# Optimization experiments

Hardware: AMD Instinct MI355X
Metric: run time of the kernel (lower is better)

Reference implementation:

```python
import jax, jax.numpy as jnp
import numpy as np

EMB_K = 512
EMB_DIM = 256
BETA = 0.25
GAMMA = 0.99
EPS = 1e-5
B, T = 16, 4096


def setup_inputs() -> dict:
    key = jax.random.key(0)
    k1, k2, k3 = jax.random.split(key, 3)
    return {
        "inputs": jax.random.normal(k1, (B, EMB_DIM, T), dtype=jnp.float32),
        "emb_weight": jax.random.normal(k2, (EMB_K, EMB_DIM), dtype=jnp.float32),
        "ema_w": jax.random.normal(k3, (EMB_K, EMB_DIM), dtype=jnp.float32),
        "ema_cluster_size": jnp.zeros((EMB_K,), dtype=jnp.float32),
    }


def reference(inputs, emb_weight, ema_w, ema_cluster_size):
    # [B, D, T] -> [B, T, D]
    x = jnp.transpose(inputs, (0, 2, 1))
    flat = x.reshape(-1, EMB_DIM)  # [N, D]

    # squared euclidean distances to codebook: [N, K]
    dist = (jnp.sum(flat * flat, axis=1, keepdims=True)
            + jnp.sum(emb_weight * emb_weight, axis=1)
            - 2.0 * flat @ emb_weight.T)
    idx = jnp.argmin(dist, axis=1)            # [N]
    enc = jax.nn.one_hot(idx, EMB_K, dtype=flat.dtype)  # [N, K]

    # --- EMA codebook update (training branch) ---
    counts = jax.ops.segment_sum(jnp.ones_like(idx, dtype=flat.dtype), idx,
                                 num_segments=EMB_K)  # == enc.sum(0)
    new_cs = ema_cluster_size * GAMMA + (1.0 - GAMMA) * counts
    n = jnp.sum(new_cs)
    new_cs = (new_cs + EPS) / (n + EMB_K * EPS) * n
    dw = jax.ops.segment_sum(flat, idx, num_segments=EMB_K)  # == enc.T @ flat
    new_ema_w = ema_w * GAMMA + (1.0 - GAMMA) * dw
    new_emb_weight = new_ema_w / new_cs[:, None]

    # quantize with updated codebook (gather == enc @ new_emb_weight)
    Q = new_emb_weight[idx].reshape(x.shape)  # [B, T, D]

    e_latent_loss = jnp.mean((jax.lax.stop_gradient(Q) - x) ** 2)
    loss = BETA * e_latent_loss

    # straight-through
    Q_st = x + jax.lax.stop_gradient(Q - x)

    avg_probs = jnp.mean(enc, axis=0)
    PP = jnp.exp(-jnp.sum(avg_probs * jnp.log(avg_probs + 1e-10)))

    return loss, jnp.transpose(Q_st, (0, 2, 1)), PP, enc
```

## Files before the change

### kernel.cpp

```cpp
#include <hip/hip_runtime.h>

#define N_TOT 65536
#define DIM 256
#define KK 512
#define TT 4096
#define BB 16

typedef short bf16x8 __attribute__((ext_vector_type(8)));
typedef float f32x4 __attribute__((ext_vector_type(4)));

__device__ __forceinline__ ushort f2bf(float f) {
    unsigned u = __float_as_uint(f);
    unsigned r = (u + 0x7fffu + ((u >> 16) & 1u)) >> 16;
    return (ushort)r;
}

__global__ void k_se(const float* __restrict__ emb, float* __restrict__ se) {
    int wid = threadIdx.x >> 6, lane = threadIdx.x & 63;
    int k = blockIdx.x * 4 + wid;
    const float4* e4 = (const float4*)emb;
    float4 v = e4[k * 64 + lane];
    float s = v.x * v.x + v.y * v.y + v.z * v.z + v.w * v.w;
#pragma unroll
    for (int m = 1; m < 64; m <<= 1) s += __shfl_xor(s, m);
    if (lane == 0) se[k] = s;
}

__global__ void k_split_e(const float* __restrict__ emb, ushort* __restrict__ eb) {
    int k = blockIdx.x, tid = threadIdx.x;
    int c0 = tid * 4;
    float4 v = *(const float4*)(emb + k * DIM + c0);
    float f[4] = {v.x, v.y, v.z, v.w};
    ushort h[4], l[4];
#pragma unroll
    for (int j = 0; j < 4; ++j) {
        h[j] = f2bf(f[j]);
        float hf = __uint_as_float(((unsigned)h[j]) << 16);
        l[j] = f2bf(f[j] - hf);
    }
    uint2 hp = make_uint2((unsigned)h[0] | ((unsigned)h[1] << 16),
                          (unsigned)h[2] | ((unsigned)h[3] << 16));
    uint2 lp = make_uint2((unsigned)l[0] | ((unsigned)l[1] << 16),
                          (unsigned)l[2] | ((unsigned)l[3] << 16));
    *(uint2*)(eb + (size_t)k * 512 + c0) = hp;
    *(uint2*)(eb + (size_t)k * 512 + 256 + c0) = lp;
}

__global__ __launch_bounds__(256) void k_split_x(const float* __restrict__ in,
                                                 ushort* __restrict__ xt) {
    __shared__ float ls[64][65];
    int tid = threadIdx.x;
    int b = blockIdx.x >> 8;
    int rest = blockIdx.x & 255;
    int tt = rest >> 2, dt = rest & 3;
    int t0 = tt * 64, d0 = dt * 64;
    int tl = tid & 63, dg = tid >> 6;
    const float* src = in + (size_t)b * DIM * TT + t0 + tl;
#pragma unroll
    for (int p = 0; p < 16; ++p) {
        int d = dg * 16 + p;
        ls[d][tl] = src[(size_t)(d0 + d) * TT];
    }
    __syncthreads();
    int c0 = dg * 16;
    int n = b * TT + t0 + tl;
    ushort* row = xt + (size_t)n * 512;
    ushort h[16], l[16];
#pragma unroll
    for (int j = 0; j < 16; ++j) {
        float v = ls[c0 + j][tl];
        h[j] = f2bf(v);
        float hf = __uint_as_float(((unsigned)h[j]) << 16);
        l[j] = f2bf(v - hf);
    }
    uint hu[8], lu[8];
#pragma unroll
    for (int j = 0; j < 8; ++j) {
        hu[j] = (unsigned)h[2 * j] | ((unsigned)h[2 * j + 1] << 16);
        lu[j] = (unsigned)l[2 * j] | ((unsigned)l[2 * j + 1] << 16);
    }
    *(uint4*)(row + d0 + c0) = make_uint4(hu[0], hu[1], hu[2], hu[3]);
    *(uint4*)(row + d0 + c0 + 8) = make_uint4(hu[4], hu[5], hu[6], hu[7]);
    *(uint4*)(row + 256 + d0 + c0) = make_uint4(lu[0], lu[1], lu[2], lu[3]);
    *(uint4*)(row + 256 + d0 + c0 + 8) = make_uint4(lu[4], lu[5], lu[6], lu[7]);
}

__global__ void k_zero(float* __restrict__ dw, unsigned* __restrict__ counts,
                       unsigned* __restrict__ lossd) {
    int i = blockIdx.x * 256 + threadIdx.x;
    if (i < 131072) dw[i] = 0.f;
    int j = i - 131072;
    if (j >= 0 && j < 512) counts[j] = 0u;
    if (j >= 512 && j < 514) lossd[j - 512] = 0u;
}

__global__ __launch_bounds__(256) void k_dist(
    const ushort* __restrict__ xt, const ushort* __restrict__ eb,
    const float* __restrict__ se,
    float* __restrict__ partd, int* __restrict__ parti) {
    __shared__ ushort As[128 * 64];
    __shared__ ushort Bs[128 * 64];
    const int tid = threadIdx.x;
    const int lane = tid & 63, w = tid >> 6;
    const int bj = blockIdx.x, bi = blockIdx.y;
    const int n0 = bi * 128, k0 = bj * 128;
    const int wr = w >> 1, wc = w & 1;

    f32x4 acc[4][4] = {};

    for (int it = 0; it < 12; ++it) {
        const int region = it >> 2, sub = it & 3;
        const int aoff = (region == 2 ? 256 : 0) + sub * 64;
        const int boff = (region == 1 ? 256 : 0) + sub * 64;
#pragma unroll
        for (int i = 0; i < 4; ++i) {
            int r = i * 32 + w * 8 + (lane >> 3);
            int slot = (lane & 7) ^ (r & 7);
            const ushort* ga = xt + (size_t)(n0 + r) * 512 + aoff + slot * 8;
            const ushort* gb = eb + (size_t)(k0 + r) * 512 + boff + slot * 8;
            __builtin_amdgcn_global_load_lds(
                (const __attribute__((address_space(1))) void*)ga,
                (__attribute__((address_space(3))) void*)&As[(size_t)(i * 256 + w * 64) * 8],
                16, 0, 0);
            __builtin_amdgcn_global_load_lds(
                (const __attribute__((address_space(1))) void*)gb,
                (__attribute__((address_space(3))) void*)&Bs[(size_t)(i * 256 + w * 64) * 8],
                16, 0, 0);
        }
        __syncthreads();
#pragma unroll
        for (int kk = 0; kk < 2; ++kk) {
            bf16x8 af[4], bfr[4];
#pragma unroll
            for (int mi = 0; mi < 4; ++mi) {
                int row = wr * 64 + mi * 16 + (lane & 15);
                int slot = (kk * 4 + (lane >> 4)) ^ (row & 7);
                af[mi] = *(const bf16x8*)&As[row * 64 + slot * 8];
            }
#pragma unroll
            for (int ni = 0; ni < 4; ++ni) {
                int row = wc * 64 + ni * 16 + (lane & 15);
                int slot = (kk * 4 + (lane >> 4)) ^ (row & 7);
                bfr[ni] = *(const bf16x8*)&Bs[row * 64 + slot * 8];
            }
#pragma unroll
            for (int mi = 0; mi < 4; ++mi)
#pragma unroll
                for (int ni = 0; ni < 4; ++ni)
                    acc[mi][ni] = __builtin_amdgcn_mfma_f32_16x16x32_bf16(
                        af[mi], bfr[ni], acc[mi][ni], 0, 0, 0);
        }
        __syncthreads();
    }

    float* pd = (float*)As;
    int* pi = (int*)Bs;
#pragma unroll
    for (int mi = 0; mi < 4; ++mi) {
#pragma unroll
        for (int j = 0; j < 4; ++j) {
            int r = wr * 64 + mi * 16 + (lane >> 4) * 4 + j;
            float dmin = 3.4e38f;
            int bidx = 0x7fffffff;
#pragma unroll
            for (int ni = 0; ni < 4; ++ni) {
                int k = k0 + wc * 64 + ni * 16 + (lane & 15);
                float dv = fmaf(-2.f, acc[mi][ni][j], se[k]);
                if (dv < dmin) { dmin = dv; bidx = k; }
            }
            pd[r * 32 + wc * 16 + (lane & 15)] = dmin;
            pi[r * 32 + wc * 16 + (lane & 15)] = bidx;
        }
    }
    __syncthreads();
    if (tid < 128) {
        float dmin = 3.4e38f;
        int bidx = 0x7fffffff;
        for (int c = 0; c < 32; ++c) {
            float dv = pd[tid * 32 + c];
            int iv = pi[tid * 32 + c];
            if (dv < dmin || (dv == dmin && iv < bidx)) { dmin = dv; bidx = iv; }
        }
        partd[(size_t)bj * N_TOT + n0 + tid] = dmin;
        parti[(size_t)bj * N_TOT + n0 + tid] = bidx;
    }
}

__global__ void k_combine(const float* __restrict__ partd, const int* __restrict__ parti,
                          int* __restrict__ idx, unsigned* __restrict__ counts) {
    __shared__ unsigned h[512];
    int tid = threadIdx.x;
    h[tid] = 0u;
    h[tid + 256] = 0u;
    __syncthreads();
    int n = blockIdx.x * 256 + tid;
    float dmin = 3.4e38f;
    int bidx = 0x7fffffff;
#pragma unroll
    for (int p = 0; p < 4; ++p) {
        float dv = partd[(size_t)p * N_TOT + n];
        int iv = parti[(size_t)p * N_TOT + n];
        if (dv < dmin || (dv == dmin && iv < bidx)) { dmin = dv; bidx = iv; }
    }
    idx[n] = bidx;
    atomicAdd(&h[bidx], 1u);
    __syncthreads();
    if (h[tid]) atomicAdd(&counts[tid], h[tid]);
    if (h[tid + 256]) atomicAdd(&counts[tid + 256], h[tid + 256]);
}

__global__ void k_enc_zero(float2* __restrict__ enc2) {
    size_t base = (size_t)blockIdx.x * (256 * 32) + threadIdx.x;
#pragma unroll
    for (int j = 0; j < 32; ++j) enc2[base + j * 256] = make_float2(0.f, 0.f);
}

__global__ void k_enc_ones(const int* __restrict__ idx, float* __restrict__ enc) {
    int n = blockIdx.x * 256 + threadIdx.x;
    enc[(size_t)n * KK + idx[n]] = 1.0f;
}

__global__ void k_scalars(const unsigned* __restrict__ counts, const float* __restrict__ cs_in,
                          float* __restrict__ csn, float* __restrict__ pp_out,
                          unsigned* __restrict__ cursor) {
    __shared__ float red[512];
    __shared__ unsigned sc[512];
    int k = threadIdx.x;
    unsigned ci = counts[k];
    float c = (float)ci;
    float pre = cs_in[k] * 0.99f + 0.01f * c;
    red[k] = pre;
    sc[k] = ci;
    __syncthreads();
#pragma unroll
    for (int s = 256; s > 0; s >>= 1) {
        if (k < s) red[k] += red[k + s];
        __syncthreads();
    }
    float nsum = red[0];
    __syncthreads();
    csn[k] = (pre + 1e-5f) / (nsum + 512 * 1e-5f) * nsum;
    float p = c * (1.0f / 65536.f);
    red[k] = -p * logf(p + 1e-10f);
    __syncthreads();
#pragma unroll
    for (int s = 256; s > 0; s >>= 1) {
        if (k < s) red[k] += red[k + s];
        __syncthreads();
    }
    if (k == 0) pp_out[0] = expf(red[0]);
#pragma unroll
    for (int s = 1; s < 512; s <<= 1) {
        unsigned v = (k >= s) ? sc[k - s] : 0u;
        __syncthreads();
        sc[k] += v;
        __syncthreads();
    }
    cursor[k] = sc[k] - ci;
}

__global__ void k_scatter(const int* __restrict__ idx, unsigned* __restrict__ cursor,
                          unsigned* __restrict__ sortedp) {
    int n = blockIdx.x * 256 + threadIdx.x;
    int k = idx[n];
    unsigned p = atomicAdd(&cursor[k], 1u);
    sortedp[p] = (unsigned)n | ((unsigned)k << 17);
}

__global__ __launch_bounds__(256) void k_dwsum(const ushort* __restrict__ xt,
                                               const unsigned* __restrict__ sortedp,
                                               float* __restrict__ dw) {
    int gw = blockIdx.x * 4 + (threadIdx.x >> 6);
    int lane = threadIdx.x & 63;
    int base = gw * 16;
    unsigned pk[16];
#pragma unroll
    for (int i = 0; i < 16; ++i) pk[i] = sortedp[base + i];
    float acc[8] = {0.f, 0.f, 0.f, 0.f, 0.f, 0.f, 0.f, 0.f};
    int curk = (int)(pk[0] >> 17);
#pragma unroll
    for (int i = 0; i < 16; ++i) {
        int n = (int)(pk[i] & 0x1ffffu);
        int k = (int)(pk[i] >> 17);
        if (k != curk) {
#pragma unroll
            for (int j = 0; j < 8; ++j) {
                float other = __shfl(acc[j], lane + 32);
                if (lane < 32) atomicAdd(&dw[curk * DIM + lane * 8 + j], acc[j] + other);
                acc[j] = 0.f;
            }
            curk = k;
        }
        uint4 v = *(const uint4*)(xt + (size_t)n * 512 + lane * 8);
        unsigned u[4] = {v.x, v.y, v.z, v.w};
#pragma unroll
        for (int j = 0; j < 4; ++j) {
            acc[2 * j] += __uint_as_float(u[j] << 16);
            acc[2 * j + 1] += __uint_as_float(u[j] & 0xffff0000u);
        }
    }
#pragma unroll
    for (int j = 0; j < 8; ++j) {
        float other = __shfl(acc[j], lane + 32);
        if (lane < 32) atomicAdd(&dw[curk * DIM + lane * 8 + j], acc[j] + other);
    }
}

__global__ void k_newemb(const float* __restrict__ ema_w, const float* __restrict__ dw,
                         const float* __restrict__ csn, float* __restrict__ newemb) {
    int i = blockIdx.x * 256 + threadIdx.x;
    int k = i >> 8;
    newemb[i] = (ema_w[i] * 0.99f + 0.01f * dw[i]) / csn[k];
}

__global__ __launch_bounds__(256) void k_out1(const float* __restrict__ in,
                                              const int* __restrict__ idx,
                                              const float* __restrict__ newemb,
                                              float* __restrict__ out1,
                                              unsigned long long* __restrict__ lossd) {
    __shared__ float q[256][68];
    __shared__ float redl[4];
    int tid = threadIdx.x;
    int b = blockIdx.x >> 6, tc = blockIdx.x & 63;
    int tl = tid & 63, dg = tid >> 6;
    int kk = idx[b * TT + tc * 64 + tl];
    const float4* ne4 = (const float4*)(newemb + (size_t)kk * DIM);
#pragma unroll
    for (int d4 = 0; d4 < 16; ++d4) {
        float4 v = ne4[dg * 16 + d4];
        int d = dg * 64 + d4 * 4;
        q[d + 0][tl] = v.x;
        q[d + 1][tl] = v.y;
        q[d + 2][tl] = v.z;
        q[d + 3][tl] = v.w;
    }
    __syncthreads();
    float lacc = 0.f;
    const float* xb = in + (size_t)b * DIM * TT + tc * 64;
    float* ob = out1 + (size_t)b * DIM * TT + tc * 64;
#pragma unroll 4
    for (int j = 0; j < 64; ++j) {
        int fi = tid + 256 * j;
        int d = fi >> 6, t = fi & 63;
        float qv = q[d][t];
        float xv = xb[(size_t)d * TT + t];
        ob[(size_t)d * TT + t] = qv;
        float df = qv - xv;
        lacc = fmaf(df, df, lacc);
    }
#pragma unroll
    for (int m = 1; m < 64; m <<= 1) lacc += __shfl_xor(lacc, m);
    if ((tid & 63) == 0) redl[tid >> 6] = lacc;
    __syncthreads();
    if (tid == 0) {
        double s = (double)redl[0] + (double)redl[1] + (double)redl[2] + (double)redl[3];
        atomicAdd((double*)lossd, s);
    }
}

__global__ void k_loss_fin(const double* __restrict__ lossd, float* __restrict__ out0) {
    out0[0] = (float)(0.25 * lossd[0] * (1.0 / 16777216.0));
}

extern "C" void kernel_launch(void* const* d_in, const int* in_sizes, int n_in,
                              void* d_out, int out_size, void* d_ws, size_t ws_size,
                              hipStream_t stream) {
    const float* in = (const float*)d_in[0];
    const float* emb = (const float*)d_in[1];
    const float* emaw = (const float*)d_in[2];
    const float* cs = (const float*)d_in[3];
    float* out = (float*)d_out;
    char* ws = (char*)d_ws;

    float* se = (float*)(ws + 0);
    float* partd = (float*)(ws + 264192);
    int* parti = (int*)(ws + 1312768);
    int* idx = (int*)(ws + 2361344);
    unsigned* counts = (unsigned*)(ws + 2623488);
    float* csn = (float*)(ws + 2625536);
    float* dw = (float*)(ws + 2627584);
    float* newemb = (float*)(ws + 3151872);
    double* lossd = (double*)(ws + 3676160);
    ushort* eb = (ushort*)(ws + 3676416);
    ushort* xt = (ushort*)(ws + 4200704);
    unsigned* sortedp = (unsigned*)(ws + 71309568);
    unsigned* cursor = (unsigned*)(ws + 71573760);

    float* out_loss = out;
    float* out_q = out + 1;
    float* out_pp = out + 16777217;
    float* enc = out + 16777218;

    hipLaunchKernelGGL(k_se, dim3(128), dim3(256), 0, stream, emb, se);
    hipLaunchKernelGGL(k_split_e, dim3(512), dim3(64), 0, stream, emb, eb);
    hipLaunchKernelGGL(k_split_x, dim3(4096), dim3(256), 0, stream, in, xt);
    hipLaunchKernelGGL(k_zero, dim3(515), dim3(256), 0, stream, dw, counts, (unsigned*)lossd);
    hipLaunchKernelGGL(k_dist, dim3(4, 512), dim3(256), 0, stream, xt, eb, se, partd, parti);
    hipLaunchKernelGGL(k_combine, dim3(256), dim3(256), 0, stream, partd, parti, idx, counts);
    hipLaunchKernelGGL(k_enc_zero, dim3(2048), dim3(256), 0, stream, (float2*)enc);
    hipLaunchKernelGGL(k_enc_ones, dim3(256), dim3(256), 0, stream, idx, enc);
    hipLaunchKernelGGL(k_scalars, dim3(1), dim3(512), 0, stream, counts, cs, csn, out_pp, cursor);
    hipLaunchKernelGGL(k_scatter, dim3(256), dim3(256), 0, stream, idx, cursor, sortedp);
    hipLaunchKernelGGL(k_dwsum, dim3(1024), dim3(256), 0, stream, xt, sortedp, dw);
    hipLaunchKernelGGL(k_newemb, dim3(512), dim3(256), 0, stream, emaw, dw, csn, newemb);
    hipLaunchKernelGGL(k_out1, dim3(1024), dim3(256), 0, stream, in, idx, newemb, out_q,
                       (unsigned long long*)lossd);
    hipLaunchKernelGGL(k_loss_fin, dim3(1), dim3(1), 0, stream, lossd, out_loss);
}
```

Baseline: 376.2 us.

## Double-buffer dist GEMM tiles, fuse one-hot writes, split loss off output pass

The distance GEMM now uses two LDS buffers so the next K-slice's global-to-LDS loads are issued before computing on the current one, removing one barrier per iteration. The separate zero and scatter-ones kernels for the one-hot encoding are merged into a single kernel that writes each row once with vector stores. The loss reduction moves out of the quantized-output kernel into its own kernel, which reads the bf16 hi/lo split of x instead of re-reading the fp32 input, so the output pass becomes pure stores. Trade-offs are doubled LDS per block, which may cut occupancy, and an extra launch for the loss.

```diff
diff --git a/kernel.cpp b/kernel.cpp
--- a/kernel.cpp
+++ b/kernel.cpp
@@ -98,8 +98,8 @@
     const ushort* __restrict__ xt, const ushort* __restrict__ eb,
     const float* __restrict__ se,
     float* __restrict__ partd, int* __restrict__ parti) {
-    __shared__ ushort As[128 * 64];
-    __shared__ ushort Bs[128 * 64];
+    __shared__ ushort As[2][8192];
+    __shared__ ushort Bs[2][8192];
     const int tid = threadIdx.x;
     const int lane = tid & 63, w = tid >> 6;
     const int bj = blockIdx.x, bi = blockIdx.y;
@@ -108,26 +108,35 @@
 
     f32x4 acc[4][4] = {};
 
+    const int r_st = w * 8 + (lane >> 3);
+    const int s_st = lane & 7;
+
+#define STAGE(IT, B)                                                          \
+    do {                                                                      \
+        const int region = (IT) >> 2, sub = (IT) & 3;                         \
+        const int aoff = (region == 2 ? 256 : 0) + sub * 64;                  \
+        const int boff = (region == 1 ? 256 : 0) + sub * 64;                  \
+        _Pragma("unroll") for (int i = 0; i < 4; ++i) {                       \
+            int r = i * 32 + r_st;                                            \
+            int slot = s_st ^ (r & 7);                                        \
+            const ushort* ga = xt + (size_t)(n0 + r) * 512 + aoff + slot * 8; \
+            const ushort* gb = eb + (size_t)(k0 + r) * 512 + boff + slot * 8; \
+            __builtin_amdgcn_global_load_lds(                                 \
+                (const __attribute__((address_space(1))) void*)ga,            \
+                (__attribute__((address_space(3))) void*)&As[B][(i * 256 + w * 64) * 8], \
+                16, 0, 0);                                                    \
+            __builtin_amdgcn_global_load_lds(                                 \
+                (const __attribute__((address_space(1))) void*)gb,            \
+                (__attribute__((address_space(3))) void*)&Bs[B][(i * 256 + w * 64) * 8], \
+                16, 0, 0);                                                    \
+        }                                                                     \
+    } while (0)
+
+    STAGE(0, 0);
+    __syncthreads();
     for (int it = 0; it < 12; ++it) {
-        const int region = it >> 2, sub = it & 3;
-        const int aoff = (region == 2 ? 256 : 0) + sub * 64;
-        const int boff = (region == 1 ? 256 : 0) + sub * 64;
-#pragma unroll
-        for (int i = 0; i < 4; ++i) {
-            int r = i * 32 + w * 8 + (lane >> 3);
-            int slot = (lane & 7) ^ (r & 7);
-            const ushort* ga = xt + (size_t)(n0 + r) * 512 + aoff + slot * 8;
-            const ushort* gb = eb + (size_t)(k0 + r) * 512 + boff + slot * 8;
-            __builtin_amdgcn_global_load_lds(
-                (const __attribute__((address_space(1))) void*)ga,
-                (__attribute__((address_space(3))) void*)&As[(size_t)(i * 256 + w * 64) * 8],
-                16, 0, 0);
-            __builtin_amdgcn_global_load_lds(
-                (const __attribute__((address_space(1))) void*)gb,
-                (__attribute__((address_space(3))) void*)&Bs[(size_t)(i * 256 + w * 64) * 8],
-                16, 0, 0);
-        }
-        __syncthreads();
+        const int buf = it & 1;
+        if (it < 11) STAGE(it + 1, buf ^ 1);
 #pragma unroll
         for (int kk = 0; kk < 2; ++kk) {
             bf16x8 af[4], bfr[4];
@@ -135,13 +144,13 @@
             for (int mi = 0; mi < 4; ++mi) {
                 int row = wr * 64 + mi * 16 + (lane & 15);
                 int slot = (kk * 4 + (lane >> 4)) ^ (row & 7);
-                af[mi] = *(const bf16x8*)&As[row * 64 + slot * 8];
+                af[mi] = *(const bf16x8*)&As[buf][row * 64 + slot * 8];
             }
 #pragma unroll
             for (int ni = 0; ni < 4; ++ni) {
                 int row = wc * 64 + ni * 16 + (lane & 15);
                 int slot = (kk * 4 + (lane >> 4)) ^ (row & 7);
-                bfr[ni] = *(const bf16x8*)&Bs[row * 64 + slot * 8];
+                bfr[ni] = *(const bf16x8*)&Bs[buf][row * 64 + slot * 8];
             }
 #pragma unroll
             for (int mi = 0; mi < 4; ++mi)
@@ -152,9 +161,10 @@
         }
         __syncthreads();
     }
-
-    float* pd = (float*)As;
-    int* pi = (int*)Bs;
+#undef STAGE
+
+    float* pd = (float*)&As[0][0];
+    int* pi = (int*)&Bs[0][0];
 #pragma unroll
     for (int mi = 0; mi < 4; ++mi) {
 #pragma unroll
@@ -209,15 +219,23 @@
     if (h[tid + 256]) atomicAdd(&counts[tid + 256], h[tid + 256]);
 }
 
-__global__ void k_enc_zero(float2* __restrict__ enc2) {
-    size_t base = (size_t)blockIdx.x * (256 * 32) + threadIdx.x;
-#pragma unroll
-    for (int j = 0; j < 32; ++j) enc2[base + j * 256] = make_float2(0.f, 0.f);
-}
-
-__global__ void k_enc_ones(const int* __restrict__ idx, float* __restrict__ enc) {
-    int n = blockIdx.x * 256 + threadIdx.x;
-    enc[(size_t)n * KK + idx[n]] = 1.0f;
+__global__ __launch_bounds__(256) void k_enc(const int* __restrict__ idx,
+                                             float* __restrict__ enc) {
+    int w = threadIdx.x >> 6, lane = threadIdx.x & 63;
+    int row0 = blockIdx.x * 64 + w * 16;
+#pragma unroll 4
+    for (int r = 0; r < 16; ++r) {
+        int n = row0 + r;
+        int k = idx[n];
+        int hit = (lane == (k >> 3));
+        int kj = k & 7;
+        float v[8];
+#pragma unroll
+        for (int j = 0; j < 8; ++j) v[j] = (hit && (kj == j)) ? 1.0f : 0.0f;
+        float* p = enc + (size_t)n * KK + lane * 8;
+        *(float4*)p = make_float4(v[0], v[1], v[2], v[3]);
+        *(float4*)(p + 4) = make_float4(v[4], v[5], v[6], v[7]);
+    }
 }
 
 __global__ void k_scalars(const unsigned* __restrict__ counts, const float* __restrict__ cs_in,
@@ -313,13 +331,10 @@
     newemb[i] = (ema_w[i] * 0.99f + 0.01f * dw[i]) / csn[k];
 }
 
-__global__ __launch_bounds__(256) void k_out1(const float* __restrict__ in,
-                                              const int* __restrict__ idx,
+__global__ __launch_bounds__(256) void k_out1(const int* __restrict__ idx,
                                               const float* __restrict__ newemb,
-                                              float* __restrict__ out1,
-                                              unsigned long long* __restrict__ lossd) {
+                                              float* __restrict__ out1) {
     __shared__ float q[256][68];
-    __shared__ float redl[4];
     int tid = threadIdx.x;
     int b = blockIdx.x >> 6, tc = blockIdx.x & 63;
     int tl = tid & 63, dg = tid >> 6;
@@ -335,27 +350,42 @@
         q[d + 3][tl] = v.w;
     }
     __syncthreads();
-    float lacc = 0.f;
-    const float* xb = in + (size_t)b * DIM * TT + tc * 64;
     float* ob = out1 + (size_t)b * DIM * TT + tc * 64;
-#pragma unroll 4
+#pragma unroll 8
     for (int j = 0; j < 64; ++j) {
         int fi = tid + 256 * j;
         int d = fi >> 6, t = fi & 63;
-        float qv = q[d][t];
-        float xv = xb[(size_t)d * TT + t];
-        ob[(size_t)d * TT + t] = qv;
-        float df = qv - xv;
-        lacc = fmaf(df, df, lacc);
-    }
-#pragma unroll
-    for (int m = 1; m < 64; m <<= 1) lacc += __shfl_xor(lacc, m);
-    if ((tid & 63) == 0) redl[tid >> 6] = lacc;
-    __syncthreads();
-    if (tid == 0) {
-        double s = (double)redl[0] + (double)redl[1] + (double)redl[2] + (double)redl[3];
-        atomicAdd((double*)lossd, s);
-    }
+        ob[(size_t)d * TT + t] = q[d][t];
+    }
+}
+
+__global__ __launch_bounds__(256) void k_loss(const ushort* __restrict__ xt,
+                                              const int* __restrict__ idx,
+                                              const float* __restrict__ newemb,
+                                              double* __restrict__ lossd) {
+    int gw = blockIdx.x * 4 + (threadIdx.x >> 6);
+    int lane = threadIdx.x & 63;
+    float acc = 0.f;
+    for (int i = 0; i < 64; ++i) {
+        int n = gw * 64 + i;
+        int k = idx[n];
+        const ushort* row = xt + (size_t)n * 512;
+        uint2 h2 = *(const uint2*)(row + lane * 4);
+        uint2 l2 = *(const uint2*)(row + 256 + lane * 4);
+        float4 qv = *(const float4*)(newemb + (size_t)k * DIM + lane * 4);
+        float x0 = __uint_as_float(h2.x << 16) + __uint_as_float(l2.x << 16);
+        float x1 = __uint_as_float(h2.x & 0xffff0000u) + __uint_as_float(l2.x & 0xffff0000u);
+        float x2 = __uint_as_float(h2.y << 16) + __uint_as_float(l2.y << 16);
+        float x3 = __uint_as_float(h2.y & 0xffff0000u) + __uint_as_float(l2.y & 0xffff0000u);
+        float d0 = qv.x - x0, d1 = qv.y - x1, d2 = qv.z - x2, d3 = qv.w - x3;
+        acc = fmaf(d0, d0, acc);
+        acc = fmaf(d1, d1, acc);
+        acc = fmaf(d2, d2, acc);
+        acc = fmaf(d3, d3, acc);
+    }
+#pragma unroll
+    for (int m = 1; m < 64; m <<= 1) acc += __shfl_xor(acc, m);
+    if (lane == 0) atomicAdd(lossd, (double)acc);
 }
 
 __global__ void k_loss_fin(const double* __restrict__ lossd, float* __restrict__ out0) {
@@ -397,13 +427,12 @@
     hipLaunchKernelGGL(k_zero, dim3(515), dim3(256), 0, stream, dw, counts, (unsigned*)lossd);
     hipLaunchKernelGGL(k_dist, dim3(4, 512), dim3(256), 0, stream, xt, eb, se, partd, parti);
     hipLaunchKernelGGL(k_combine, dim3(256), dim3(256), 0, stream, partd, parti, idx, counts);
-    hipLaunchKernelGGL(k_enc_zero, dim3(2048), dim3(256), 0, stream, (float2*)enc);
-    hipLaunchKernelGGL(k_enc_ones, dim3(256), dim3(256), 0, stream, idx, enc);
+    hipLaunchKernelGGL(k_enc, dim3(1024), dim3(256), 0, stream, idx, enc);
     hipLaunchKernelGGL(k_scalars, dim3(1), dim3(512), 0, stream, counts, cs, csn, out_pp, cursor);
     hipLaunchKernelGGL(k_scatter, dim3(256), dim3(256), 0, stream, idx, cursor, sortedp);
     hipLaunchKernelGGL(k_dwsum, dim3(1024), dim3(256), 0, stream, xt, sortedp, dw);
     hipLaunchKernelGGL(k_newemb, dim3(512), dim3(256), 0, stream, emaw, dw, csn, newemb);
-    hipLaunchKernelGGL(k_out1, dim3(1024), dim3(256), 0, stream, in, idx, newemb, out_q,
-                       (unsigned long long*)lossd);
+    hipLaunchKernelGGL(k_out1, dim3(1024), dim3(256), 0, stream, idx, newemb, out_q);
+    hipLaunchKernelGGL(k_loss, dim3(256), dim3(256), 0, stream, xt, idx, newemb, lossd);
     hipLaunchKernelGGL(k_loss_fin, dim3(1), dim3(1), 0, stream, lossd, out_loss);
 }
```

Measured after the change: 436.3 us. +16.0%, slower.
